# Performance work log

Hardware: AMD Instinct MI355X
Metric: run time of the kernel (lower is better)

Reference implementation:

```python
import jax, jax.numpy as jnp
import numpy as np

EMBED_DIM = 4096
N_HEADS = 32
N_KV_HEADS = N_HEADS // 2
HEAD_DIM = EMBED_DIM // N_HEADS
MAX_SEQ_LEN = 4096


def setup_inputs() -> dict:
    key = jax.random.key(0)
    k1, k2, k3, k4, k5 = jax.random.split(key, 5)
    b, s = 1, 2048
    x = jax.random.normal(k1, (b, s, EMBED_DIM), dtype=jnp.float32)
    # rotary frequencies: theta=10000, angles[t, i] = t * 10000^{-2i/head_dim}
    inv_freq = 1.0 / (10000.0 ** (np.arange(0, HEAD_DIM, 2, dtype=np.float32) / HEAD_DIM))
    t = np.arange(MAX_SEQ_LEN, dtype=np.float32)
    ang = np.outer(t, inv_freq)  # [max_seq, head_dim/2]
    freqs_cis = jnp.asarray(np.stack([np.cos(ang), np.sin(ang)], axis=-1))  # [max_seq, hd/2, 2]
    scale = 0.02
    wq = jax.random.normal(k2, (EMBED_DIM, EMBED_DIM), dtype=jnp.float32) * scale
    wk = jax.random.normal(k3, (EMBED_DIM, N_KV_HEADS * HEAD_DIM), dtype=jnp.float32) * scale
    wv = jax.random.normal(k4, (EMBED_DIM, N_KV_HEADS * HEAD_DIM), dtype=jnp.float32) * scale
    wo = jax.random.normal(k5, (EMBED_DIM, EMBED_DIM), dtype=jnp.float32) * scale
    return {"x": x, "freqs_cis": freqs_cis, "wq": wq, "wk": wk, "wv": wv, "wo": wo, "start_pos": 0}


def _apply_rope(t, cos, sin):
    # t: [b, s, h, hd]; cos/sin: [1, s, 1, hd/2]
    tr = t.reshape(*t.shape[:-1], HEAD_DIM // 2, 2)
    t0, t1 = tr[..., 0], tr[..., 1]
    o0 = t0 * cos - t1 * sin
    o1 = t0 * sin + t1 * cos
    return jnp.stack([o0, o1], axis=-1).reshape(t.shape)


def reference(x, freqs_cis, wq, wk, wv, wo, start_pos):
    b, s, _ = x.shape
    q = (x @ wq).reshape(b, s, N_HEADS, HEAD_DIM)
    k = (x @ wk).reshape(b, s, N_KV_HEADS, HEAD_DIM)
    v = (x @ wv).reshape(b, s, N_KV_HEADS, HEAD_DIM)
    rep = N_HEADS // N_KV_HEADS
    k = jnp.repeat(k, rep, axis=2)  # GQA: expand KV heads (matches repeat_interleave)
    v = jnp.repeat(v, rep, axis=2)
    fc = freqs_cis[start_pos:start_pos + s]  # [s, hd/2, 2]
    cos = fc[None, :, None, :, 0]
    sin = fc[None, :, None, :, 1]
    q = _apply_rope(q, cos, sin)
    k = _apply_rope(k, cos, sin)
    # [b, h, s, hd]
    q = q.transpose(0, 2, 1, 3)
    k = k.transpose(0, 2, 1, 3)
    v = v.transpose(0, 2, 1, 3)
    scale = 1.0 / jnp.sqrt(jnp.float32(HEAD_DIM))
    scores = jnp.einsum("bhqd,bhkd->bhqk", q, k) * scale
    causal = jnp.tril(jnp.ones((s, s), dtype=bool))
    scores = jnp.where(causal[None, None], scores, jnp.finfo(scores.dtype).min)
    probs = jax.nn.softmax(scores, axis=-1)
    out = jnp.einsum("bhqk,bhkd->bhqd", probs, v)
    out = out.transpose(0, 2, 1, 3).reshape(b, s, EMBED_DIM)
    return out @ wo
```

## Files before the change

kernel.cpp:

```cpp
#include <hip/hip_runtime.h>
#include <stdint.h>

typedef unsigned short u16;
typedef __bf16 bf16x8 __attribute__((ext_vector_type(8)));
typedef float f32x4 __attribute__((ext_vector_type(4)));

#define SEQ   2048
#define EMBED 4096
#define KDIM  4096
#define NH    32
#define NKV   16
#define HD    128
#define KVW   2048

__device__ __forceinline__ float bf2f(u16 u) {
  union { uint32_t u; float f; } v; v.u = ((uint32_t)u) << 16; return v.f;
}
__device__ __forceinline__ u16 f2bf(float f) {
  union { float f; uint32_t u; } v; v.f = f;
  return (u16)((v.u + 0x7FFFu + ((v.u >> 16) & 1u)) >> 16);
}
__device__ __forceinline__ void g2l16(const u16* g, u16* l) {
  __builtin_amdgcn_global_load_lds(
      (const __attribute__((address_space(1))) uint32_t*)g,
      (__attribute__((address_space(3))) uint32_t*)l, 16, 0, 0);
}

__global__ __launch_bounds__(256) void convert_x(
    const float* __restrict__ X, u16* __restrict__ Xb, int nquad) {
  for (int i = blockIdx.x * 256 + threadIdx.x; i < nquad;
       i += gridDim.x * 256) {
    float4 v = *(const float4*)(X + (size_t)i * 4);
    ushort4 o;
    o.x = f2bf(v.x); o.y = f2bf(v.y); o.z = f2bf(v.z); o.w = f2bf(v.w);
    *(ushort4*)(Xb + (size_t)i * 4) = o;
  }
}

__global__ __launch_bounds__(256) void transpose_cvt(
    const float* __restrict__ W, u16* __restrict__ Wt, int K, int N) {
  __shared__ u16 tile[64][68];
  const int t = threadIdx.x;
  const int n0 = blockIdx.x * 64, k0 = blockIdx.y * 64;
#pragma unroll
  for (int i = 0; i < 4; i++) {
    int c = i * 256 + t;
    int r = c >> 4, cq = c & 15;
    float4 v = *(const float4*)(W + (size_t)(k0 + r) * N + n0 + cq * 4);
    tile[r][cq * 4 + 0] = f2bf(v.x); tile[r][cq * 4 + 1] = f2bf(v.y);
    tile[r][cq * 4 + 2] = f2bf(v.z); tile[r][cq * 4 + 3] = f2bf(v.w);
  }
  __syncthreads();
#pragma unroll
  for (int i = 0; i < 4; i++) {
    int c = i * 256 + t;
    int rn = c >> 4, cq = c & 15;
    ushort4 v;
    v.x = tile[cq * 4 + 0][rn];
    v.y = tile[cq * 4 + 1][rn];
    v.z = tile[cq * 4 + 2][rn];
    v.w = tile[cq * 4 + 3][rn];
    *(ushort4*)(Wt + (size_t)(n0 + rn) * K + k0 + cq * 4) = v;
  }
}

__global__ __launch_bounds__(512, 2) void gemm8_qkv(
    const u16* __restrict__ A,
    const u16* __restrict__ B0, const u16* __restrict__ B1,
    const u16* __restrict__ B2,
    u16* __restrict__ Qo, u16* __restrict__ Ko, u16* __restrict__ Vt) {
  __shared__ __align__(16) u16 As[2][256 * 64];
  __shared__ __align__(16) u16 Bs[2][256 * 64];
  const int t = threadIdx.x;
  const int lane = t & 63;
  const int w = t >> 6;
  const int wr = w >> 2;
  const int wc = w & 3;
  const int g = lane >> 4;
  const int l15 = lane & 15;

  const int bid = blockIdx.x;
  const int swz = (bid & 7) * 32 + (bid >> 3);
  const int mb = swz & 7;
  const int nb = swz >> 3;
  const int m0 = mb * 256;

  const u16* Bt; int nrow0;
  if (nb < 16)      { Bt = B0; nrow0 = nb * 256; }
  else if (nb < 24) { Bt = B1; nrow0 = (nb - 16) * 256; }
  else              { Bt = B2; nrow0 = (nb - 24) * 256; }

  auto stageA = [&](int buf, int kt, int h) {
#pragma unroll
    for (int i = 0; i < 2; i++) {
      int c = i * 512 + t;
      int row = c >> 3, sp = c & 7;
      int col = (sp ^ (row & 7)) << 3;
      g2l16(A + (size_t)(m0 + h * 128 + row) * KDIM + kt + col,
            &As[buf][h * 8192 + c * 8]);
    }
  };
  auto stageB = [&](int buf, int kt, int h) {
#pragma unroll
    for (int i = 0; i < 2; i++) {
      int c = i * 512 + t;
      int row = c >> 3, sp = c & 7;
      int col = (sp ^ (row & 7)) << 3;
      g2l16(Bt + (size_t)(nrow0 + h * 128 + row) * KDIM + kt + col,
            &Bs[buf][h * 8192 + c * 8]);
    }
  };

  f32x4 acc[8][4];
#pragma unroll
  for (int i = 0; i < 8; i++)
#pragma unroll
    for (int j = 0; j < 4; j++) acc[i][j] = (f32x4){0.f, 0.f, 0.f, 0.f};

  stageA(0, 0, 0); stageA(0, 0, 1);
  stageB(0, 0, 0); stageB(0, 0, 1);
  stageA(1, 64, 0); stageA(1, 64, 1);
  stageB(1, 64, 0); stageB(1, 64, 1);
  asm volatile("s_waitcnt vmcnt(8)" ::: "memory");
  __builtin_amdgcn_s_barrier();

  const int NT = KDIM / 64;
  for (int ti = 0; ti < NT; ++ti) {
    const int cur = ti & 1;
    const u16* Asc = As[cur];
    const u16* Bsc = Bs[cur];
    const int ktn2 = (ti + 2) * 64;
    bf16x8 a0[2][4], a1[2][4], b0[2][2], b1[2][2];

#pragma unroll
    for (int kk = 0; kk < 2; kk++)
#pragma unroll
      for (int mi = 0; mi < 4; mi++) {
        int r = wr * 128 + mi * 16 + l15;
        int slot = (kk * 4 + g) ^ (r & 7);
        a0[kk][mi] = *(const bf16x8*)(Asc + r * 64 + slot * 8);
      }
#pragma unroll
    for (int kk = 0; kk < 2; kk++)
#pragma unroll
      for (int ni = 0; ni < 2; ni++) {
        int r = wc * 64 + ni * 16 + l15;
        int slot = (kk * 4 + g) ^ (r & 7);
        b0[kk][ni] = *(const bf16x8*)(Bsc + r * 64 + slot * 8);
      }
    __builtin_amdgcn_s_barrier();
    asm volatile("s_waitcnt lgkmcnt(0)" ::: "memory");
    __builtin_amdgcn_sched_barrier(0);
    __builtin_amdgcn_s_setprio(1);
#pragma unroll
    for (int mi = 0; mi < 4; mi++)
#pragma unroll
      for (int ni = 0; ni < 2; ni++)
#pragma unroll
        for (int kk = 0; kk < 2; kk++)
          acc[mi][ni] = __builtin_amdgcn_mfma_f32_16x16x32_bf16(
              a0[kk][mi], b0[kk][ni], acc[mi][ni], 0, 0, 0);
    __builtin_amdgcn_s_setprio(0);
    __builtin_amdgcn_s_barrier();

#pragma unroll
    for (int kk = 0; kk < 2; kk++)
#pragma unroll
      for (int mi = 0; mi < 4; mi++) {
        int r = wr * 128 + 64 + mi * 16 + l15;
        int slot = (kk * 4 + g) ^ (r & 7);
        a1[kk][mi] = *(const bf16x8*)(Asc + r * 64 + slot * 8);
      }
    __builtin_amdgcn_s_barrier();
    asm volatile("s_waitcnt lgkmcnt(0)" ::: "memory");
    __builtin_amdgcn_sched_barrier(0);
    __builtin_amdgcn_s_setprio(1);
#pragma unroll
    for (int mi = 0; mi < 4; mi++)
#pragma unroll
      for (int ni = 0; ni < 2; ni++)
#pragma unroll
        for (int kk = 0; kk < 2; kk++)
          acc[mi + 4][ni] = __builtin_amdgcn_mfma_f32_16x16x32_bf16(
              a1[kk][mi], b0[kk][ni], acc[mi + 4][ni], 0, 0, 0);
    __builtin_amdgcn_s_setprio(0);
    __builtin_amdgcn_s_barrier();

#pragma unroll
    for (int kk = 0; kk < 2; kk++)
#pragma unroll
      for (int ni = 0; ni < 2; ni++) {
        int r = wc * 64 + (ni + 2) * 16 + l15;
        int slot = (kk * 4 + g) ^ (r & 7);
        b1[kk][ni] = *(const bf16x8*)(Bsc + r * 64 + slot * 8);
      }
    if (ti + 2 < NT) { stageA(cur, ktn2, 0); stageA(cur, ktn2, 1); }
    __builtin_amdgcn_s_barrier();
    asm volatile("s_waitcnt lgkmcnt(0)" ::: "memory");
    __builtin_amdgcn_sched_barrier(0);
    __builtin_amdgcn_s_setprio(1);
#pragma unroll
    for (int mi = 0; mi < 4; mi++)
#pragma unroll
      for (int ni = 0; ni < 2; ni++)
#pragma unroll
        for (int kk = 0; kk < 2; kk++)
          acc[mi + 4][ni + 2] = __builtin_amdgcn_mfma_f32_16x16x32_bf16(
              a1[kk][mi], b1[kk][ni], acc[mi + 4][ni + 2], 0, 0, 0);
    __builtin_amdgcn_s_setprio(0);
    __builtin_amdgcn_s_barrier();

    if (ti + 2 < NT) { stageB(cur, ktn2, 0); stageB(cur, ktn2, 1); }
    __builtin_amdgcn_s_barrier();
    __builtin_amdgcn_s_setprio(1);
#pragma unroll
    for (int mi = 0; mi < 4; mi++)
#pragma unroll
      for (int ni = 0; ni < 2; ni++)
#pragma unroll
        for (int kk = 0; kk < 2; kk++)
          acc[mi][ni + 2] = __builtin_amdgcn_mfma_f32_16x16x32_bf16(
              a0[kk][mi], b1[kk][ni], acc[mi][ni + 2], 0, 0, 0);
    __builtin_amdgcn_s_setprio(0);
    if (ti + 2 < NT)      asm volatile("s_waitcnt vmcnt(8)" ::: "memory");
    else if (ti + 1 < NT) asm volatile("s_waitcnt vmcnt(0)" ::: "memory");
    __builtin_amdgcn_s_barrier();
  }

#pragma unroll
  for (int mi = 0; mi < 8; mi++) {
#pragma unroll
    for (int ni = 0; ni < 4; ni++) {
      int rowg = m0 + wr * 128 + mi * 16 + g * 4;
      int ncol = nb * 256 + wc * 64 + ni * 16 + l15;
      if (nb < 16) {
#pragma unroll
        for (int r = 0; r < 4; r++)
          Qo[(size_t)(rowg + r) * EMBED + ncol] = f2bf(acc[mi][ni][r]);
      } else if (nb < 24) {
        int nc = ncol - 4096;
#pragma unroll
        for (int r = 0; r < 4; r++)
          Ko[(size_t)(rowg + r) * KVW + nc] = f2bf(acc[mi][ni][r]);
      } else {
        int nc = ncol - 6144;
        ushort4 v;
        v.x = f2bf(acc[mi][ni][0]); v.y = f2bf(acc[mi][ni][1]);
        v.z = f2bf(acc[mi][ni][2]); v.w = f2bf(acc[mi][ni][3]);
        *(ushort4*)(Vt + (size_t)nc * SEQ + rowg) = v;
      }
    }
  }
}

__global__ __launch_bounds__(512, 2) void gemm8_op(
    const u16* __restrict__ A, const u16* __restrict__ Bt,
    float* __restrict__ Cf) {
  __shared__ __align__(16) u16 As[2][128 * 64];
  __shared__ __align__(16) u16 Bs[2][256 * 64];
  const int t = threadIdx.x;
  const int lane = t & 63;
  const int w = t >> 6;
  const int wr = w >> 2;
  const int wc = w & 3;
  const int g = lane >> 4;
  const int l15 = lane & 15;

  const int bid = blockIdx.x;
  const int swz = (bid & 7) * 32 + (bid >> 3);
  const int mb = swz & 15;
  const int nb = swz >> 4;
  const int m0 = mb * 128;
  const int nrow0 = nb * 256;

  auto stageA = [&](int buf, int kt) {
#pragma unroll
    for (int i = 0; i < 2; i++) {
      int c = i * 512 + t;
      int row = c >> 3, sp = c & 7;
      int col = (sp ^ (row & 7)) << 3;
      g2l16(A + (size_t)(m0 + row) * KDIM + kt + col, &As[buf][c * 8]);
    }
  };
  auto stageB = [&](int buf, int kt) {
#pragma unroll
    for (int i = 0; i < 4; i++) {
      int c = i * 512 + t;
      int row = c >> 3, sp = c & 7;
      int col = (sp ^ (row & 7)) << 3;
      g2l16(Bt + (size_t)(nrow0 + row) * KDIM + kt + col, &Bs[buf][c * 8]);
    }
  };

  f32x4 acc[4][4];
#pragma unroll
  for (int i = 0; i < 4; i++)
#pragma unroll
    for (int j = 0; j < 4; j++) acc[i][j] = (f32x4){0.f, 0.f, 0.f, 0.f};

  stageA(0, 0); stageB(0, 0);
  stageA(1, 64); stageB(1, 64);
  asm volatile("s_waitcnt vmcnt(6)" ::: "memory");
  __builtin_amdgcn_s_barrier();

  const int NT = KDIM / 64;
  for (int ti = 0; ti < NT; ++ti) {
    const int cur = ti & 1;
    const u16* Asc = As[cur];
    const u16* Bsc = Bs[cur];
    const int ktn2 = (ti + 2) * 64;
    bf16x8 a[2][4], b0[2][2], b1[2][2];

#pragma unroll
    for (int kk = 0; kk < 2; kk++)
#pragma unroll
      for (int mi = 0; mi < 4; mi++) {
        int r = wr * 64 + mi * 16 + l15;
        int slot = (kk * 4 + g) ^ (r & 7);
        a[kk][mi] = *(const bf16x8*)(Asc + r * 64 + slot * 8);
      }
#pragma unroll
    for (int kk = 0; kk < 2; kk++)
#pragma unroll
      for (int ni = 0; ni < 2; ni++) {
        int r = wc * 64 + ni * 16 + l15;
        int slot = (kk * 4 + g) ^ (r & 7);
        b0[kk][ni] = *(const bf16x8*)(Bsc + r * 64 + slot * 8);
      }
#pragma unroll
    for (int kk = 0; kk < 2; kk++)
#pragma unroll
      for (int ni = 0; ni < 2; ni++) {
        int r = wc * 64 + (ni + 2) * 16 + l15;
        int slot = (kk * 4 + g) ^ (r & 7);
        b1[kk][ni] = *(const bf16x8*)(Bsc + r * 64 + slot * 8);
      }
    __builtin_amdgcn_s_barrier();
    asm volatile("s_waitcnt lgkmcnt(0)" ::: "memory");
    __builtin_amdgcn_sched_barrier(0);
    __builtin_amdgcn_s_setprio(1);
#pragma unroll
    for (int mi = 0; mi < 4; mi++)
#pragma unroll
      for (int ni = 0; ni < 2; ni++)
#pragma unroll
        for (int kk = 0; kk < 2; kk++)
          acc[mi][ni] = __builtin_amdgcn_mfma_f32_16x16x32_bf16(
              a[kk][mi], b0[kk][ni], acc[mi][ni], 0, 0, 0);
    __builtin_amdgcn_s_setprio(0);
    __builtin_amdgcn_s_barrier();

    if (ti + 2 < NT) { stageA(cur, ktn2); stageB(cur, ktn2); }
    __builtin_amdgcn_s_barrier();
    __builtin_amdgcn_s_setprio(1);
#pragma unroll
    for (int mi = 0; mi < 4; mi++)
#pragma unroll
      for (int ni = 0; ni < 2; ni++)
#pragma unroll
        for (int kk = 0; kk < 2; kk++)
          acc[mi][ni + 2] = __builtin_amdgcn_mfma_f32_16x16x32_bf16(
              a[kk][mi], b1[kk][ni], acc[mi][ni + 2], 0, 0, 0);
    __builtin_amdgcn_s_setprio(0);
    if (ti + 2 < NT)      asm volatile("s_waitcnt vmcnt(6)" ::: "memory");
    else if (ti + 1 < NT) asm volatile("s_waitcnt vmcnt(0)" ::: "memory");
    __builtin_amdgcn_s_barrier();
  }

#pragma unroll
  for (int mi = 0; mi < 4; mi++)
#pragma unroll
    for (int ni = 0; ni < 4; ni++) {
      int rowg = m0 + wr * 64 + mi * 16 + g * 4;
      int ncol = nb * 256 + wc * 64 + ni * 16 + l15;
#pragma unroll
      for (int r = 0; r < 4; r++)
        Cf[(size_t)(rowg + r) * 4096 + ncol] = acc[mi][ni][r];
    }
}

__global__ __launch_bounds__(256) void rope_kernel(
    u16* __restrict__ Q, u16* __restrict__ Kb,
    const float* __restrict__ freqs, const int* __restrict__ start_pos) {
  const int sp = start_pos[0];
  const float qscale = 0.08838834764831845f;
  const int total_q = SEQ * EMBED / 2;
  const int total_k = SEQ * KVW / 2;
  const int total = total_q + total_k;
  for (int idx = blockIdx.x * 256 + threadIdx.x; idx < total;
       idx += gridDim.x * 256) {
    u16* buf; int row, pi; bool isq = idx < total_q;
    if (isq) { row = idx >> 11; pi = idx & 2047; buf = Q + (size_t)row * EMBED; }
    else { int j = idx - total_q; row = j >> 10; pi = j & 1023; buf = Kb + (size_t)row * KVW; }
    int i = pi & 63;
    float2 cs = *(const float2*)(freqs + (size_t)(sp + row) * 128 + i * 2);
    float c = cs.x, s = cs.y;
    ushort2 tv = *(ushort2*)(buf + pi * 2);
    float t0 = bf2f(tv.x), t1 = bf2f(tv.y);
    float o0 = t0 * c - t1 * s;
    float o1 = t0 * s + t1 * c;
    if (isq) { o0 *= qscale; o1 *= qscale; }
    ushort2 o; o.x = f2bf(o0); o.y = f2bf(o1);
    *(ushort2*)(buf + pi * 2) = o;
  }
}

__global__ __launch_bounds__(256, 4) void attn_kernel(
    const u16* __restrict__ Q, const u16* __restrict__ Kb,
    const u16* __restrict__ Vt, u16* __restrict__ O) {
  __shared__ __align__(16) u16 KV[16384];
  __shared__ u16 Ps[4][16 * 72];

  const int t = threadIdx.x;
  const int lane = t & 63;
  const int w = t >> 6;
  const int g = lane >> 4;
  const int l15 = lane & 15;
  const int bid = blockIdx.x;
  const int qb = 31 - (bid >> 5);
  const int h = bid & 31;
  const int hk = h >> 1;

  auto stageK = [&](int kv) {
#pragma unroll
    for (int i = 0; i < 4; i++) {
      int c = i * 256 + t;
      int row = c >> 4, spp = c & 15;
      int col = ((spp ^ (row & 7)) << 3);
      g2l16(Kb + (size_t)(kv * 64 + row) * KVW + hk * HD + col, &KV[c * 8]);
    }
  };
  auto stageV = [&](int kv) {
#pragma unroll
    for (int i = 0; i < 4; i++) {
      int c = i * 256 + t;
      int row = c >> 3, spp = c & 7;
      int col = ((spp ^ (row & 7)) << 3);
      g2l16(Vt + (size_t)(hk * HD + row) * SEQ + kv * 64 + col,
            &KV[8192 + c * 8]);
    }
  };

#pragma unroll
  for (int i = 0; i < 4; i++) {
    int c = i * 256 + t;
    int row = c >> 4, spp = c & 15;
    int col = ((spp ^ (row & 7)) << 3);
    g2l16(Q + (size_t)(qb * 64 + row) * EMBED + h * HD + col, &KV[c * 8]);
  }
  asm volatile("s_waitcnt vmcnt(0)" ::: "memory");
  __builtin_amdgcn_s_barrier();

  bf16x8 qf[4];
  {
    int r = w * 16 + l15;
#pragma unroll
    for (int kk = 0; kk < 4; kk++) {
      int ps = (kk * 4 + g) ^ (r & 7);
      qf[kk] = *(const bf16x8*)(&KV[r * 128 + ps * 8]);
    }
  }
  asm volatile("s_waitcnt lgkmcnt(0)" ::: "memory");
  __builtin_amdgcn_s_barrier();

  f32x4 oacc[8];
#pragma unroll
  for (int i = 0; i < 8; i++) oacc[i] = (f32x4){0.f, 0.f, 0.f, 0.f};
  float mrow = -1e30f, lrow = 0.f;
  const int qg = qb * 64 + w * 16 + l15;

  for (int kv = 0; kv <= qb; kv++) {
    stageK(kv); stageV(kv);
    asm volatile("s_waitcnt vmcnt(0)" ::: "memory");
    __builtin_amdgcn_s_barrier();

    f32x4 sfragT[4];
    __builtin_amdgcn_s_setprio(1);
#pragma unroll
    for (int ni = 0; ni < 4; ni++) {
      f32x4 s = (f32x4){0.f, 0.f, 0.f, 0.f};
      int r = ni * 16 + l15;
#pragma unroll
      for (int kk = 0; kk < 4; kk++) {
        int ps = (kk * 4 + g) ^ (r & 7);
        bf16x8 a = *(const bf16x8*)(&KV[r * 128 + ps * 8]);
        s = __builtin_amdgcn_mfma_f32_16x16x32_bf16(a, qf[kk], s, 0, 0, 0);
      }
      sfragT[ni] = s;
    }
    __builtin_amdgcn_s_setprio(0);

    if (kv == qb) {
#pragma unroll
      for (int ni = 0; ni < 4; ni++) {
        int colg = kv * 64 + ni * 16 + g * 4;
#pragma unroll
        for (int r = 0; r < 4; r++)
          if (colg + r > qg) sfragT[ni][r] = -1e30f;
      }
    }

    float m16 = sfragT[0][0];
#pragma unroll
    for (int ni = 0; ni < 4; ni++)
#pragma unroll
      for (int r = 0; r < 4; r++) m16 = fmaxf(m16, sfragT[ni][r]);
    m16 = fmaxf(m16, __shfl_xor(m16, 16));
    m16 = fmaxf(m16, __shfl_xor(m16, 32));
    float mnew = fmaxf(mrow, m16);
    float sc = __expf(mrow - mnew);
    mrow = mnew;

    float rsum = 0.f;
#pragma unroll
    for (int ni = 0; ni < 4; ni++) {
#pragma unroll
      for (int r = 0; r < 4; r++) {
        float p = __expf(sfragT[ni][r] - mrow);
        rsum += p;
        Ps[w][l15 * 72 + ni * 16 + g * 4 + r] = f2bf(p);
      }
    }
    rsum += __shfl_xor(rsum, 16);
    rsum += __shfl_xor(rsum, 32);
    lrow = lrow * sc + rsum;

    float scr[4];
#pragma unroll
    for (int r = 0; r < 4; r++) scr[r] = __shfl(sc, g * 4 + r, 64);
#pragma unroll
    for (int nf = 0; nf < 8; nf++)
#pragma unroll
      for (int r = 0; r < 4; r++) oacc[nf][r] *= scr[r];

    asm volatile("s_waitcnt lgkmcnt(0)" ::: "memory");

    bf16x8 pa[2];
#pragma unroll
    for (int kk = 0; kk < 2; kk++)
      pa[kk] = *(const bf16x8*)(&Ps[w][l15 * 72 + kk * 32 + g * 8]);
    __builtin_amdgcn_s_setprio(1);
#pragma unroll
    for (int nf = 0; nf < 8; nf++) {
      int r = nf * 16 + l15;
#pragma unroll
      for (int kk = 0; kk < 2; kk++) {
        int ps = (kk * 4 + g) ^ (r & 7);
        bf16x8 b = *(const bf16x8*)(&KV[8192 + r * 64 + ps * 8]);
        oacc[nf] = __builtin_amdgcn_mfma_f32_16x16x32_bf16(pa[kk], b, oacc[nf], 0, 0, 0);
      }
    }
    __builtin_amdgcn_s_setprio(0);
    __builtin_amdgcn_s_barrier();
  }

  float lr[4];
#pragma unroll
  for (int r = 0; r < 4; r++) lr[r] = __shfl(lrow, g * 4 + r, 64);
#pragma unroll
  for (int nf = 0; nf < 8; nf++) {
#pragma unroll
    for (int r = 0; r < 4; r++) {
      int rowg = qb * 64 + w * 16 + g * 4 + r;
      float v = oacc[nf][r] / lr[r];
      O[(size_t)rowg * EMBED + h * HD + nf * 16 + l15] = f2bf(v);
    }
  }
}

extern "C" void kernel_launch(void* const* d_in, const int* in_sizes, int n_in,
                              void* d_out, int out_size, void* d_ws, size_t ws_size,
                              hipStream_t stream) {
  const float* x  = (const float*)d_in[0];
  const float* fc = (const float*)d_in[1];
  const float* wq = (const float*)d_in[2];
  const float* wk = (const float*)d_in[3];
  const float* wv = (const float*)d_in[4];
  const float* wo = (const float*)d_in[5];
  const int* sp = (const int*)d_in[6];

  char* ws = (char*)d_ws;
  u16* wqT = (u16*)(ws);
  u16* wkT = (u16*)(ws + 33554432ull);
  u16* wvT = (u16*)(ws + 50331648ull);
  u16* woT = (u16*)(ws + 67108864ull);
  u16* xb  = (u16*)(ws + 100663296ull);
  u16* Qb  = (u16*)(ws + 117440512ull);
  u16* Kb  = (u16*)(ws + 134217728ull);
  u16* Vt  = (u16*)(ws + 142606336ull);
  u16* Ob  = (u16*)(ws + 150994944ull);

  convert_x<<<dim3(2048), 256, 0, stream>>>(x, xb, SEQ * EMBED / 4);
  transpose_cvt<<<dim3(64, 64), 256, 0, stream>>>(wq, wqT, 4096, 4096);
  transpose_cvt<<<dim3(32, 64), 256, 0, stream>>>(wk, wkT, 4096, 2048);
  transpose_cvt<<<dim3(32, 64), 256, 0, stream>>>(wv, wvT, 4096, 2048);
  transpose_cvt<<<dim3(64, 64), 256, 0, stream>>>(wo, woT, 4096, 4096);

  gemm8_qkv<<<dim3(256), 512, 0, stream>>>(xb, wqT, wkT, wvT, Qb, Kb, Vt);
  rope_kernel<<<dim3(2048), 256, 0, stream>>>(Qb, Kb, fc, sp);
  attn_kernel<<<dim3(1024), 256, 0, stream>>>(Qb, Kb, Vt, Ob);
  gemm8_op<<<dim3(256), 512, 0, stream>>>(Ob, woT, (float*)d_out);
}
```

Baseline: 360.5 us.

## Simplify GEMM pipeline to single-barrier prefetch-one-ahead double buffering

Replaces the interleaved multi-phase schedule, which issued the two-ahead prefetch between MFMA groups with several barriers per K-tile, with a simpler loop. Each iteration waits for all global loads, takes one barrier, prefetches the next tile into the other buffer, then loads all LDS fragments and runs every MFMA back to back. Launch bounds change from 2 to 1 block per CU, which lets the compiler use more registers. The aim is lower barrier overhead, at the risk of exposing global load latency now that prefetch is only one tile ahead, and of lower occupancy.

```diff
diff --git a/kernel.cpp b/kernel.cpp
--- a/kernel.cpp
+++ b/kernel.cpp
@@ -24,6 +24,11 @@
   __builtin_amdgcn_global_load_lds(
       (const __attribute__((address_space(1))) uint32_t*)g,
       (__attribute__((address_space(3))) uint32_t*)l, 16, 0, 0);
+}
+__device__ __forceinline__ void BAR() {
+  asm volatile("" ::: "memory");
+  __builtin_amdgcn_s_barrier();
+  asm volatile("" ::: "memory");
 }
 
 __global__ __launch_bounds__(256) void convert_x(
@@ -64,7 +69,7 @@
   }
 }
 
-__global__ __launch_bounds__(512, 2) void gemm8_qkv(
+__global__ __launch_bounds__(512, 1) void gemm8_qkv(
     const u16* __restrict__ A,
     const u16* __restrict__ B0, const u16* __restrict__ B1,
     const u16* __restrict__ B2,
@@ -78,6 +83,7 @@
   const int wc = w & 3;
   const int g = lane >> 4;
   const int l15 = lane & 15;
+  const int NT = KDIM / 64;
 
   const int bid = blockIdx.x;
   const int swz = (bid & 7) * 32 + (bid >> 3);
@@ -90,7 +96,7 @@
   else if (nb < 24) { Bt = B1; nrow0 = (nb - 16) * 256; }
   else              { Bt = B2; nrow0 = (nb - 24) * 256; }
 
-  auto stageA = [&](int buf, int kt, int h) {
+  auto stA = [&](int buf, int kt, int h) {
 #pragma unroll
     for (int i = 0; i < 2; i++) {
       int c = i * 512 + t;
@@ -100,7 +106,7 @@
             &As[buf][h * 8192 + c * 8]);
     }
   };
-  auto stageB = [&](int buf, int kt, int h) {
+  auto stB = [&](int buf, int kt, int h) {
 #pragma unroll
     for (int i = 0; i < 2; i++) {
       int c = i * 512 + t;
@@ -117,40 +123,51 @@
 #pragma unroll
     for (int j = 0; j < 4; j++) acc[i][j] = (f32x4){0.f, 0.f, 0.f, 0.f};
 
-  stageA(0, 0, 0); stageA(0, 0, 1);
-  stageB(0, 0, 0); stageB(0, 0, 1);
-  stageA(1, 64, 0); stageA(1, 64, 1);
-  stageB(1, 64, 0); stageB(1, 64, 1);
-  asm volatile("s_waitcnt vmcnt(8)" ::: "memory");
-  __builtin_amdgcn_s_barrier();
-
-  const int NT = KDIM / 64;
+  stA(0, 0, 0); stA(0, 0, 1); stB(0, 0, 0); stB(0, 0, 1);
+
   for (int ti = 0; ti < NT; ++ti) {
     const int cur = ti & 1;
     const u16* Asc = As[cur];
     const u16* Bsc = Bs[cur];
-    const int ktn2 = (ti + 2) * 64;
+    const int kt1 = (ti + 1) * 64;
+
+    asm volatile("s_waitcnt vmcnt(0)" ::: "memory");
+    BAR();
+    if (ti + 1 < NT) {
+      stA(cur ^ 1, kt1, 0); stA(cur ^ 1, kt1, 1);
+      stB(cur ^ 1, kt1, 0); stB(cur ^ 1, kt1, 1);
+    }
     bf16x8 a0[2][4], a1[2][4], b0[2][2], b1[2][2];
-
-#pragma unroll
-    for (int kk = 0; kk < 2; kk++)
+#pragma unroll
+    for (int kk = 0; kk < 2; kk++) {
 #pragma unroll
       for (int mi = 0; mi < 4; mi++) {
-        int r = wr * 128 + mi * 16 + l15;
-        int slot = (kk * 4 + g) ^ (r & 7);
-        a0[kk][mi] = *(const bf16x8*)(Asc + r * 64 + slot * 8);
-      }
-#pragma unroll
-    for (int kk = 0; kk < 2; kk++)
+        int r0 = wr * 128 + mi * 16 + l15;
+        int s0 = (kk * 4 + g) ^ (r0 & 7);
+        a0[kk][mi] = *(const bf16x8*)(Asc + r0 * 64 + s0 * 8);
+      }
 #pragma unroll
       for (int ni = 0; ni < 2; ni++) {
-        int r = wc * 64 + ni * 16 + l15;
-        int slot = (kk * 4 + g) ^ (r & 7);
-        b0[kk][ni] = *(const bf16x8*)(Bsc + r * 64 + slot * 8);
-      }
-    __builtin_amdgcn_s_barrier();
-    asm volatile("s_waitcnt lgkmcnt(0)" ::: "memory");
-    __builtin_amdgcn_sched_barrier(0);
+        int r0 = wc * 64 + ni * 16 + l15;
+        int s0 = (kk * 4 + g) ^ (r0 & 7);
+        b0[kk][ni] = *(const bf16x8*)(Bsc + r0 * 64 + s0 * 8);
+      }
+    }
+#pragma unroll
+    for (int kk = 0; kk < 2; kk++) {
+#pragma unroll
+      for (int mi = 0; mi < 4; mi++) {
+        int r1 = wr * 128 + 64 + mi * 16 + l15;
+        int s1 = (kk * 4 + g) ^ (r1 & 7);
+        a1[kk][mi] = *(const bf16x8*)(Asc + r1 * 64 + s1 * 8);
+      }
+#pragma unroll
+      for (int ni = 0; ni < 2; ni++) {
+        int r1 = wc * 64 + (ni + 2) * 16 + l15;
+        int s1 = (kk * 4 + g) ^ (r1 & 7);
+        b1[kk][ni] = *(const bf16x8*)(Bsc + r1 * 64 + s1 * 8);
+      }
+    }
     __builtin_amdgcn_s_setprio(1);
 #pragma unroll
     for (int mi = 0; mi < 4; mi++)
@@ -160,21 +177,6 @@
         for (int kk = 0; kk < 2; kk++)
           acc[mi][ni] = __builtin_amdgcn_mfma_f32_16x16x32_bf16(
               a0[kk][mi], b0[kk][ni], acc[mi][ni], 0, 0, 0);
-    __builtin_amdgcn_s_setprio(0);
-    __builtin_amdgcn_s_barrier();
-
-#pragma unroll
-    for (int kk = 0; kk < 2; kk++)
-#pragma unroll
-      for (int mi = 0; mi < 4; mi++) {
-        int r = wr * 128 + 64 + mi * 16 + l15;
-        int slot = (kk * 4 + g) ^ (r & 7);
-        a1[kk][mi] = *(const bf16x8*)(Asc + r * 64 + slot * 8);
-      }
-    __builtin_amdgcn_s_barrier();
-    asm volatile("s_waitcnt lgkmcnt(0)" ::: "memory");
-    __builtin_amdgcn_sched_barrier(0);
-    __builtin_amdgcn_s_setprio(1);
 #pragma unroll
     for (int mi = 0; mi < 4; mi++)
 #pragma unroll
@@ -183,22 +185,6 @@
         for (int kk = 0; kk < 2; kk++)
           acc[mi + 4][ni] = __builtin_amdgcn_mfma_f32_16x16x32_bf16(
               a1[kk][mi], b0[kk][ni], acc[mi + 4][ni], 0, 0, 0);
-    __builtin_amdgcn_s_setprio(0);
-    __builtin_amdgcn_s_barrier();
-
-#pragma unroll
-    for (int kk = 0; kk < 2; kk++)
-#pragma unroll
-      for (int ni = 0; ni < 2; ni++) {
-        int r = wc * 64 + (ni + 2) * 16 + l15;
-        int slot = (kk * 4 + g) ^ (r & 7);
-        b1[kk][ni] = *(const bf16x8*)(Bsc + r * 64 + slot * 8);
-      }
-    if (ti + 2 < NT) { stageA(cur, ktn2, 0); stageA(cur, ktn2, 1); }
-    __builtin_amdgcn_s_barrier();
-    asm volatile("s_waitcnt lgkmcnt(0)" ::: "memory");
-    __builtin_amdgcn_sched_barrier(0);
-    __builtin_amdgcn_s_setprio(1);
 #pragma unroll
     for (int mi = 0; mi < 4; mi++)
 #pragma unroll
@@ -207,12 +193,6 @@
         for (int kk = 0; kk < 2; kk++)
           acc[mi + 4][ni + 2] = __builtin_amdgcn_mfma_f32_16x16x32_bf16(
               a1[kk][mi], b1[kk][ni], acc[mi + 4][ni + 2], 0, 0, 0);
-    __builtin_amdgcn_s_setprio(0);
-    __builtin_amdgcn_s_barrier();
-
-    if (ti + 2 < NT) { stageB(cur, ktn2, 0); stageB(cur, ktn2, 1); }
-    __builtin_amdgcn_s_barrier();
-    __builtin_amdgcn_s_setprio(1);
 #pragma unroll
     for (int mi = 0; mi < 4; mi++)
 #pragma unroll
@@ -222,9 +202,7 @@
           acc[mi][ni + 2] = __builtin_amdgcn_mfma_f32_16x16x32_bf16(
               a0[kk][mi], b1[kk][ni], acc[mi][ni + 2], 0, 0, 0);
     __builtin_amdgcn_s_setprio(0);
-    if (ti + 2 < NT)      asm volatile("s_waitcnt vmcnt(8)" ::: "memory");
-    else if (ti + 1 < NT) asm volatile("s_waitcnt vmcnt(0)" ::: "memory");
-    __builtin_amdgcn_s_barrier();
+    asm volatile("s_waitcnt lgkmcnt(0)" ::: "memory");
   }
 
 #pragma unroll
@@ -253,7 +231,7 @@
   }
 }
 
-__global__ __launch_bounds__(512, 2) void gemm8_op(
+__global__ __launch_bounds__(512, 1) void gemm8_op(
     const u16* __restrict__ A, const u16* __restrict__ Bt,
     float* __restrict__ Cf) {
   __shared__ __align__(16) u16 As[2][128 * 64];
@@ -265,6 +243,7 @@
   const int wc = w & 3;
   const int g = lane >> 4;
   const int l15 = lane & 15;
+  const int NT = KDIM / 64;
 
   const int bid = blockIdx.x;
   const int swz = (bid & 7) * 32 + (bid >> 3);
@@ -273,7 +252,7 @@
   const int m0 = mb * 128;
   const int nrow0 = nb * 256;
 
-  auto stageA = [&](int buf, int kt) {
+  auto stA = [&](int buf, int kt) {
 #pragma unroll
     for (int i = 0; i < 2; i++) {
       int c = i * 512 + t;
@@ -282,7 +261,7 @@
       g2l16(A + (size_t)(m0 + row) * KDIM + kt + col, &As[buf][c * 8]);
     }
   };
-  auto stageB = [&](int buf, int kt) {
+  auto stB = [&](int buf, int kt) {
 #pragma unroll
     for (int i = 0; i < 4; i++) {
       int c = i * 512 + t;
@@ -298,46 +277,40 @@
 #pragma unroll
     for (int j = 0; j < 4; j++) acc[i][j] = (f32x4){0.f, 0.f, 0.f, 0.f};
 
-  stageA(0, 0); stageB(0, 0);
-  stageA(1, 64); stageB(1, 64);
-  asm volatile("s_waitcnt vmcnt(6)" ::: "memory");
-  __builtin_amdgcn_s_barrier();
-
-  const int NT = KDIM / 64;
+  stA(0, 0); stB(0, 0);
+
   for (int ti = 0; ti < NT; ++ti) {
     const int cur = ti & 1;
     const u16* Asc = As[cur];
     const u16* Bsc = Bs[cur];
-    const int ktn2 = (ti + 2) * 64;
+    const int kt1 = (ti + 1) * 64;
+
+    asm volatile("s_waitcnt vmcnt(0)" ::: "memory");
+    BAR();
+    if (ti + 1 < NT) { stA(cur ^ 1, kt1); stB(cur ^ 1, kt1); }
+
     bf16x8 a[2][4], b0[2][2], b1[2][2];
-
-#pragma unroll
-    for (int kk = 0; kk < 2; kk++)
+#pragma unroll
+    for (int kk = 0; kk < 2; kk++) {
 #pragma unroll
       for (int mi = 0; mi < 4; mi++) {
         int r = wr * 64 + mi * 16 + l15;
-        int slot = (kk * 4 + g) ^ (r & 7);
-        a[kk][mi] = *(const bf16x8*)(Asc + r * 64 + slot * 8);
-      }
-#pragma unroll
-    for (int kk = 0; kk < 2; kk++)
+        int sl = (kk * 4 + g) ^ (r & 7);
+        a[kk][mi] = *(const bf16x8*)(Asc + r * 64 + sl * 8);
+      }
 #pragma unroll
       for (int ni = 0; ni < 2; ni++) {
         int r = wc * 64 + ni * 16 + l15;
-        int slot = (kk * 4 + g) ^ (r & 7);
-        b0[kk][ni] = *(const bf16x8*)(Bsc + r * 64 + slot * 8);
-      }
-#pragma unroll
-    for (int kk = 0; kk < 2; kk++)
+        int sl = (kk * 4 + g) ^ (r & 7);
+        b0[kk][ni] = *(const bf16x8*)(Bsc + r * 64 + sl * 8);
+      }
 #pragma unroll
       for (int ni = 0; ni < 2; ni++) {
         int r = wc * 64 + (ni + 2) * 16 + l15;
-        int slot = (kk * 4 + g) ^ (r & 7);
-        b1[kk][ni] = *(const bf16x8*)(Bsc + r * 64 + slot * 8);
-      }
-    __builtin_amdgcn_s_barrier();
-    asm volatile("s_waitcnt lgkmcnt(0)" ::: "memory");
-    __builtin_amdgcn_sched_barrier(0);
+        int sl = (kk * 4 + g) ^ (r & 7);
+        b1[kk][ni] = *(const bf16x8*)(Bsc + r * 64 + sl * 8);
+      }
+    }
     __builtin_amdgcn_s_setprio(1);
 #pragma unroll
     for (int mi = 0; mi < 4; mi++)
@@ -347,12 +320,6 @@
         for (int kk = 0; kk < 2; kk++)
           acc[mi][ni] = __builtin_amdgcn_mfma_f32_16x16x32_bf16(
               a[kk][mi], b0[kk][ni], acc[mi][ni], 0, 0, 0);
-    __builtin_amdgcn_s_setprio(0);
-    __builtin_amdgcn_s_barrier();
-
-    if (ti + 2 < NT) { stageA(cur, ktn2); stageB(cur, ktn2); }
-    __builtin_amdgcn_s_barrier();
-    __builtin_amdgcn_s_setprio(1);
 #pragma unroll
     for (int mi = 0; mi < 4; mi++)
 #pragma unroll
@@ -362,9 +329,7 @@
           acc[mi][ni + 2] = __builtin_amdgcn_mfma_f32_16x16x32_bf16(
               a[kk][mi], b1[kk][ni], acc[mi][ni + 2], 0, 0, 0);
     __builtin_amdgcn_s_setprio(0);
-    if (ti + 2 < NT)      asm volatile("s_waitcnt vmcnt(6)" ::: "memory");
-    else if (ti + 1 < NT) asm volatile("s_waitcnt vmcnt(0)" ::: "memory");
-    __builtin_amdgcn_s_barrier();
+    asm volatile("s_waitcnt lgkmcnt(0)" ::: "memory");
   }
 
 #pragma unroll
```

New measurement: 380.8 us. +5.6%, slower.

## Fuse RoPE into QKV GEMM epilogue and merge prep kernels into one launch

Applied to the files above, without the earlier changes.

Removes the standalone RoPE kernel by applying rotary embedding and the query scale inside the QKV GEMM epilogue. Adjacent column pairs are exchanged with a lane shuffle, and cos/sin are read per row. This avoids a full read-modify-write pass over Q and K. The x conversion and the four weight transpose-conversions are also merged into a single launch to cut launch overhead and tail gaps, at the cost of extra epilogue work and freq loads in the GEMM.

```diff
diff --git a/kernel.cpp b/kernel.cpp
--- a/kernel.cpp
+++ b/kernel.cpp
@@ -26,22 +26,33 @@
       (__attribute__((address_space(3))) uint32_t*)l, 16, 0, 0);
 }
 
-__global__ __launch_bounds__(256) void convert_x(
-    const float* __restrict__ X, u16* __restrict__ Xb, int nquad) {
-  for (int i = blockIdx.x * 256 + threadIdx.x; i < nquad;
-       i += gridDim.x * 256) {
-    float4 v = *(const float4*)(X + (size_t)i * 4);
-    ushort4 o;
-    o.x = f2bf(v.x); o.y = f2bf(v.y); o.z = f2bf(v.z); o.w = f2bf(v.w);
-    *(ushort4*)(Xb + (size_t)i * 4) = o;
-  }
-}
-
-__global__ __launch_bounds__(256) void transpose_cvt(
-    const float* __restrict__ W, u16* __restrict__ Wt, int K, int N) {
+__global__ __launch_bounds__(256) void prep_kernel(
+    const float* __restrict__ X, u16* __restrict__ Xb,
+    const float* __restrict__ wq, u16* __restrict__ wqT,
+    const float* __restrict__ wk, u16* __restrict__ wkT,
+    const float* __restrict__ wv, u16* __restrict__ wvT,
+    const float* __restrict__ wo, u16* __restrict__ woT) {
   __shared__ u16 tile[64][68];
+  int b = blockIdx.x;
   const int t = threadIdx.x;
-  const int n0 = blockIdx.x * 64, k0 = blockIdx.y * 64;
+  if (b < 2048) {
+    const int nquad = SEQ * EMBED / 4;
+    for (int i = b * 256 + t; i < nquad; i += 2048 * 256) {
+      float4 v = *(const float4*)(X + (size_t)i * 4);
+      ushort4 o;
+      o.x = f2bf(v.x); o.y = f2bf(v.y); o.z = f2bf(v.z); o.w = f2bf(v.w);
+      *(ushort4*)(Xb + (size_t)i * 4) = o;
+    }
+    return;
+  }
+  b -= 2048;
+  const float* W; u16* Wt; int N, local;
+  if (b < 4096)      { W = wq; Wt = wqT; N = 4096; local = b; }
+  else if (b < 6144) { W = wk; Wt = wkT; N = 2048; local = b - 4096; }
+  else if (b < 8192) { W = wv; Wt = wvT; N = 2048; local = b - 6144; }
+  else               { W = wo; Wt = woT; N = 4096; local = b - 8192; }
+  const int nx = N >> 6;
+  const int n0 = (local % nx) * 64, k0 = (local / nx) * 64;
 #pragma unroll
   for (int i = 0; i < 4; i++) {
     int c = i * 256 + t;
@@ -60,7 +71,7 @@
     v.y = tile[cq * 4 + 1][rn];
     v.z = tile[cq * 4 + 2][rn];
     v.w = tile[cq * 4 + 3][rn];
-    *(ushort4*)(Wt + (size_t)(n0 + rn) * K + k0 + cq * 4) = v;
+    *(ushort4*)(Wt + (size_t)(n0 + rn) * KDIM + k0 + cq * 4) = v;
   }
 }
 
@@ -68,7 +79,8 @@
     const u16* __restrict__ A,
     const u16* __restrict__ B0, const u16* __restrict__ B1,
     const u16* __restrict__ B2,
-    u16* __restrict__ Qo, u16* __restrict__ Ko, u16* __restrict__ Vt) {
+    u16* __restrict__ Qo, u16* __restrict__ Ko, u16* __restrict__ Vt,
+    const float* __restrict__ freqs, const int* __restrict__ start_pos) {
   __shared__ __align__(16) u16 As[2][256 * 64];
   __shared__ __align__(16) u16 Bs[2][256 * 64];
   const int t = threadIdx.x;
@@ -227,21 +239,30 @@
     __builtin_amdgcn_s_barrier();
   }
 
+  const int sp = start_pos[0];
+  const float qscale = 0.08838834764831845f;
 #pragma unroll
   for (int mi = 0; mi < 8; mi++) {
 #pragma unroll
     for (int ni = 0; ni < 4; ni++) {
       int rowg = m0 + wr * 128 + mi * 16 + g * 4;
       int ncol = nb * 256 + wc * 64 + ni * 16 + l15;
-      if (nb < 16) {
-#pragma unroll
-        for (int r = 0; r < 4; r++)
-          Qo[(size_t)(rowg + r) * EMBED + ncol] = f2bf(acc[mi][ni][r]);
-      } else if (nb < 24) {
-        int nc = ncol - 4096;
-#pragma unroll
-        for (int r = 0; r < 4; r++)
-          Ko[(size_t)(rowg + r) * KVW + nc] = f2bf(acc[mi][ni][r]);
+      if (nb < 24) {
+        int d = ncol & 127;
+        int i2 = d >> 1;
+        bool odd = d & 1;
+        float scale = (nb < 16) ? qscale : 1.f;
+#pragma unroll
+        for (int r = 0; r < 4; r++) {
+          float2 cs = *(const float2*)(freqs + (size_t)(sp + rowg + r) * 128 + i2 * 2);
+          float v = acc[mi][ni][r] * scale;
+          float p = __shfl_xor(v, 1);
+          float o = cs.x * v + cs.y * (odd ? p : -p);
+          if (nb < 16)
+            Qo[(size_t)(rowg + r) * EMBED + ncol] = f2bf(o);
+          else
+            Ko[(size_t)(rowg + r) * KVW + (ncol - 4096)] = f2bf(o);
+        }
       } else {
         int nc = ncol - 6144;
         ushort4 v;
@@ -379,32 +400,6 @@
     }
 }
 
-__global__ __launch_bounds__(256) void rope_kernel(
-    u16* __restrict__ Q, u16* __restrict__ Kb,
-    const float* __restrict__ freqs, const int* __restrict__ start_pos) {
-  const int sp = start_pos[0];
-  const float qscale = 0.08838834764831845f;
-  const int total_q = SEQ * EMBED / 2;
-  const int total_k = SEQ * KVW / 2;
-  const int total = total_q + total_k;
-  for (int idx = blockIdx.x * 256 + threadIdx.x; idx < total;
-       idx += gridDim.x * 256) {
-    u16* buf; int row, pi; bool isq = idx < total_q;
-    if (isq) { row = idx >> 11; pi = idx & 2047; buf = Q + (size_t)row * EMBED; }
-    else { int j = idx - total_q; row = j >> 10; pi = j & 1023; buf = Kb + (size_t)row * KVW; }
-    int i = pi & 63;
-    float2 cs = *(const float2*)(freqs + (size_t)(sp + row) * 128 + i * 2);
-    float c = cs.x, s = cs.y;
-    ushort2 tv = *(ushort2*)(buf + pi * 2);
-    float t0 = bf2f(tv.x), t1 = bf2f(tv.y);
-    float o0 = t0 * c - t1 * s;
-    float o1 = t0 * s + t1 * c;
-    if (isq) { o0 *= qscale; o1 *= qscale; }
-    ushort2 o; o.x = f2bf(o0); o.y = f2bf(o1);
-    *(ushort2*)(buf + pi * 2) = o;
-  }
-}
-
 __global__ __launch_bounds__(256, 4) void attn_kernel(
     const u16* __restrict__ Q, const u16* __restrict__ Kb,
     const u16* __restrict__ Vt, u16* __restrict__ O) {
@@ -590,14 +585,10 @@
   u16* Vt  = (u16*)(ws + 142606336ull);
   u16* Ob  = (u16*)(ws + 150994944ull);
 
-  convert_x<<<dim3(2048), 256, 0, stream>>>(x, xb, SEQ * EMBED / 4);
-  transpose_cvt<<<dim3(64, 64), 256, 0, stream>>>(wq, wqT, 4096, 4096);
-  transpose_cvt<<<dim3(32, 64), 256, 0, stream>>>(wk, wkT, 4096, 2048);
-  transpose_cvt<<<dim3(32, 64), 256, 0, stream>>>(wv, wvT, 4096, 2048);
-  transpose_cvt<<<dim3(64, 64), 256, 0, stream>>>(wo, woT, 4096, 4096);
-
-  gemm8_qkv<<<dim3(256), 512, 0, stream>>>(xb, wqT, wkT, wvT, Qb, Kb, Vt);
-  rope_kernel<<<dim3(2048), 256, 0, stream>>>(Qb, Kb, fc, sp);
+  prep_kernel<<<dim3(14336), 256, 0, stream>>>(x, xb, wq, wqT, wk, wkT,
+                                               wv, wvT, wo, woT);
+  gemm8_qkv<<<dim3(256), 512, 0, stream>>>(xb, wqT, wkT, wvT, Qb, Kb, Vt,
+                                           fc, sp);
   attn_kernel<<<dim3(1024), 256, 0, stream>>>(Qb, Kb, Vt, Ob);
   gemm8_op<<<dim3(256), 512, 0, stream>>>(Ob, woT, (float*)d_out);
 }
```

New measurement: 366.5 us. Within noise of the previous version (+1.7%).
